# Kernel tuning notes

Hardware: AMD Instinct MI355X
Metric: run time of the kernel (lower is better)

Reference implementation:

```python
import jax, jax.numpy as jnp
import numpy as np
from jax import lax

B, P, E, A, D, EMB, V, L = 16, 196, 1024, 1024, 512, 512, 10000, 32
T = L - 1  # max decode steps


def setup_inputs() -> dict:
    key = jax.random.key(0)
    ks = jax.random.split(key, 24)

    def lin(k, fan_in, shape):
        return (jax.random.normal(k, shape, jnp.float32) / np.sqrt(fan_in)).astype(jnp.float32)

    inp = {}
    inp["encoder_out"] = jax.random.normal(ks[0], (B, P, E), jnp.float32)
    # Attention (note: original builds Attention(attention_dim, decoder_dim, attention_dim),
    # so encoder_att is Linear(A, A); works because E == A)
    inp["enc_att_W"] = lin(ks[1], A, (A, A))
    inp["enc_att_b"] = jnp.zeros((A,), jnp.float32)
    inp["dec_att_W"] = lin(ks[2], D, (D, A))
    inp["dec_att_b"] = jnp.zeros((A,), jnp.float32)
    inp["full_att_W"] = lin(ks[3], A, (A, 1))
    inp["full_att_b"] = jnp.zeros((1,), jnp.float32)
    # Embedding: uniform(-0.1, 0.1) per init_weights
    inp["emb"] = jax.random.uniform(ks[4], (V, EMB), jnp.float32, -0.1, 0.1)
    # LSTMCell(embed_dim + encoder_dim, decoder_dim): gate order i, f, g, o
    inp["W_ih"] = lin(ks[5], EMB + E, (EMB + E, 4 * D))
    inp["b_ih"] = jnp.zeros((4 * D,), jnp.float32)
    inp["W_hh"] = lin(ks[6], D, (D, 4 * D))
    inp["b_hh"] = jnp.zeros((4 * D,), jnp.float32)
    inp["init_h_W"] = lin(ks[7], E, (E, D))
    inp["init_h_b"] = jnp.zeros((D,), jnp.float32)
    inp["init_c_W"] = lin(ks[8], E, (E, D))
    inp["init_c_b"] = jnp.zeros((D,), jnp.float32)
    inp["f_beta_W"] = lin(ks[9], D, (D, E))
    inp["f_beta_b"] = jnp.zeros((E,), jnp.float32)
    # fc: weight uniform(-0.1, 0.1), bias 0 per init_weights
    inp["fc_W"] = jax.random.uniform(ks[10], (D, V), jnp.float32, -0.1, 0.1)
    inp["fc_b"] = jnp.zeros((V,), jnp.float32)
    inp["encoded_captions"] = jax.random.randint(ks[11], (B, L), 0, V, jnp.int32)
    lengths = jax.random.randint(ks[12], (B,), 2, L + 1, jnp.int32)
    lengths = lengths.at[0].set(L)  # guarantee max(decode_length) == L-1 (static T)
    inp["caption_length"] = lengths[:, None]
    return inp


def reference(encoder_out, enc_att_W, enc_att_b, dec_att_W, dec_att_b,
              full_att_W, full_att_b, emb, W_ih, b_ih, W_hh, b_hh,
              init_h_W, init_h_b, init_c_W, init_c_b,
              f_beta_W, f_beta_b, fc_W, fc_b,
              encoded_captions, caption_length):
    lengths = caption_length[:, 0]
    sort_ind = jnp.argsort(-lengths, stable=True)  # descending
    lengths_s = lengths[sort_ind]
    enc = encoder_out[sort_ind]                     # [B, P, E]
    caps = encoded_captions[sort_ind]               # [B, L]
    embs = emb[caps]                                # [B, L, EMB]
    decode_len = lengths_s - 1

    mean_enc = enc.mean(axis=1)
    h0 = mean_enc @ init_h_W + init_h_b             # [B, D]
    c0 = mean_enc @ init_c_W + init_c_b

    # encoder-side attention projection is h-independent; hoist out of the loop
    att1 = enc @ enc_att_W + enc_att_b              # [B, P, A]

    def step(carry, inp_t):
        h, c = carry
        emb_t, t = inp_t
        att2 = h @ dec_att_W + dec_att_b            # [B, A]
        att = (jax.nn.relu(att1 + att2[:, None, :]) @ full_att_W)[..., 0] + full_att_b[0]  # [B, P]
        alpha = jax.nn.softmax(att, axis=1)
        awe = jnp.einsum('bpe,bp->be', enc, alpha)  # [B, E]
        gate = jax.nn.sigmoid(h @ f_beta_W + f_beta_b)
        awe = gate + awe                            # NOTE: original uses '+' (not '*')
        x = jnp.concatenate([emb_t, awe], axis=1)   # [B, EMB+E]
        gates = x @ W_ih + b_ih + h @ W_hh + b_hh   # [B, 4D]
        i, f, g, o = jnp.split(gates, 4, axis=1)
        c_new = jax.nn.sigmoid(f) * c + jax.nn.sigmoid(i) * jnp.tanh(g)
        h_new = jax.nn.sigmoid(o) * jnp.tanh(c_new)
        active = (decode_len > t)[:, None]          # ragged batch mask (== [:batch_size_t])
        h2 = jnp.where(active, h_new, h)
        c2 = jnp.where(active, c_new, c)
        preds = h_new @ fc_W + fc_b                 # dropout in eval mode (identity)
        preds = jnp.where(active, preds, 0.0)
        alpha_m = jnp.where(active, alpha, 0.0)
        return (h2, c2), (preds, alpha_m)

    xs = (embs[:, :T].transpose(1, 0, 2), jnp.arange(T))
    _, (preds, alphas) = lax.scan(step, (h0, c0), xs)
    predictions = preds.transpose(1, 0, 2)          # [B, T, V]
    alphas = alphas.transpose(1, 0, 2)              # [B, T, P]
    return predictions, caps, decode_len, alphas, sort_ind
```

## Files before the change

kernel.cpp:

```cpp
#include <hip/hip_runtime.h>
#include <math.h>

#define NB 16
#define NP 196
#define NE 1024
#define ND 512
#define NEMB 512
#define NV 10000
#define NL 32
#define NT 31
#define NG 2048

#define NBLK 256

#define OFF_PRED    0
#define OFF_CAPS    4960000
#define OFF_DECLEN  4960512
#define OFF_ALPHAS  4960528
#define OFF_SORTIND 5057744

#define OFF_ATT1B   0
#define OFF_PREIHB  1605632
#define OFF_ENCT    2113536

#define WS_LEAF   64
#define WS_H      2304
#define WS_C      10496
#define WS_M1     18688
#define WS_SCORES 84224
#define WS_AWEG   88320
#define WS_HHIST  104704

#define SMEM_BYTES 82688

__device__ __forceinline__ float sigf(float x){ return 1.0f/(1.0f+expf(-x)); }
__device__ __forceinline__ unsigned short bf16rne(float x){
  unsigned u = __float_as_uint(x);
  unsigned r = (u + 0x7fffu + ((u>>16)&1u)) >> 16;
  return (unsigned short)r;
}
__device__ __forceinline__ float bf2f(unsigned short h){ return __uint_as_float(((unsigned)h)<<16); }
__device__ __forceinline__ void u2f2(unsigned u, float&a, float&b){
  a = __uint_as_float(u<<16); b = __uint_as_float(u & 0xffff0000u);
}
__device__ __forceinline__ void cstore(float* p, float v){
  __hip_atomic_store(p, v, __ATOMIC_RELAXED, __HIP_MEMORY_SCOPE_AGENT);
}
__device__ __forceinline__ float cload(const float* p){
  return __hip_atomic_load(p, __ATOMIC_RELAXED, __HIP_MEMORY_SCOPE_AGENT);
}
__device__ __forceinline__ float2 cload2(const float* p){
  unsigned long long u = __hip_atomic_load((const unsigned long long*)p, __ATOMIC_RELAXED, __HIP_MEMORY_SCOPE_AGENT);
  float2 r; r.x = __uint_as_float((unsigned)u); r.y = __uint_as_float((unsigned)(u>>32));
  return r;
}

__global__ void k_sort(const int* __restrict__ caplen, const int* __restrict__ caps,
                       int* __restrict__ wsi, float* __restrict__ out){
  __shared__ int sidx[NB];
  int tid = threadIdx.x;
  if (tid == 0){
    int len[NB], idx[NB];
    for (int i=0;i<NB;i++){ len[i]=caplen[i]; idx[i]=i; }
    for (int i=1;i<NB;i++){
      int key=idx[i]; int kl=len[key]; int j=i-1;
      while (j>=0 && len[idx[j]]<kl){ idx[j+1]=idx[j]; j--; }
      idx[j+1]=key;
    }
    for (int b=0;b<NB;b++){
      sidx[b]=idx[b];
      wsi[b]=idx[b];
      int dl = len[idx[b]]-1;
      wsi[NB+b]=dl;
      out[OFF_DECLEN+b]=(float)dl;
      out[OFF_SORTIND+b]=(float)idx[b];
    }
  }
  __syncthreads();
  for (int x = tid; x < 2304-64; x += 64) ((unsigned*)wsi)[WS_LEAF + x] = 0u;
  for (int x=tid; x<NB*NL; x+=blockDim.x){
    int b = x>>5, l = x&31;
    out[OFF_CAPS + x] = (float)caps[sidx[b]*NL + l];
  }
}

__global__ __launch_bounds__(256) void k_mean(const float* __restrict__ enc,
                                              const int* __restrict__ wsi,
                                              float* __restrict__ wsf){
  int gid = blockIdx.x*256 + threadIdx.x;
  int b = gid>>10, e = gid&1023;
  int ob = wsi[b];
  const float* p = enc + (size_t)ob*NP*NE + e;
  float s = 0.f;
  for (int i=0;i<NP;i++) s += p[(size_t)i*NE];
  wsf[WS_M1 + b*NE + e] = s*(1.0f/196.0f);
}

__global__ __launch_bounds__(256) void k_init(const float* __restrict__ ihW, const float* __restrict__ ihb,
                                              const float* __restrict__ icW, const float* __restrict__ icb,
                                              float* __restrict__ wsf){
  int gid = blockIdx.x*256 + threadIdx.x;
  int b = gid>>10, x = gid&1023;
  int d = x&511, which = x>>9;
  const float* W = which ? icW : ihW;
  const float* mp = wsf + WS_M1 + b*NE;
  float s = which ? icb[d] : ihb[d];
  for (int e=0;e<NE;e++) s = fmaf(mp[e], W[(size_t)e*ND + d], s);
  wsf[(which?WS_C:WS_H) + b*ND + d] = s;
}

__global__ __launch_bounds__(256) void k_trans(const float* __restrict__ enc,
                                               const int* __restrict__ wsi,
                                               unsigned short* __restrict__ encT){
  __shared__ float tile[196*65];
  const int tid = threadIdx.x;
  const int b = blockIdx.x >> 4, et = blockIdx.x & 15;
  const int e0 = et*64;
  const int ob = wsi[b];
  for (int idx = tid; idx < 196*16; idx += 256){
    int p = idx >> 4, q = idx & 15;
    float4 v = *(const float4*)(enc + (size_t)ob*NP*NE + (size_t)p*NE + e0 + q*4);
    tile[p*65 + q*4+0] = v.x; tile[p*65 + q*4+1] = v.y;
    tile[p*65 + q*4+2] = v.z; tile[p*65 + q*4+3] = v.w;
  }
  __syncthreads();
  for (int idx = tid; idx < 64*52; idx += 256){
    int el = idx/52, c = idx%52;
    ushort4 o;
    int p = c*4;
    o.x = (p+0<196) ? bf16rne(tile[(p+0)*65 + el]) : (unsigned short)0;
    o.y = (p+1<196) ? bf16rne(tile[(p+1)*65 + el]) : (unsigned short)0;
    o.z = (p+2<196) ? bf16rne(tile[(p+2)*65 + el]) : (unsigned short)0;
    o.w = (p+3<196) ? bf16rne(tile[(p+3)*65 + el]) : (unsigned short)0;
    *(ushort4*)(encT + ((size_t)(b*1024 + e0 + el))*208 + c*4) = o;
  }
}

__global__ __launch_bounds__(256) void k_gemm(const void* __restrict__ Abase,
                                              const float* __restrict__ Bmat,
                                              const float* __restrict__ bias1,
                                              const float* __restrict__ bias2,
                                              void* __restrict__ outv,
                                              int M, int N, int K, int mode,
                                              int abf16, int obf16,
                                              const int* __restrict__ wsi,
                                              const int* __restrict__ caps){
  __shared__ float As[16*64];
  __shared__ float Bs[16*64];
  int tid = threadIdx.x;
  int n0 = blockIdx.x*64, m0 = blockIdx.y*64;
  int tx = tid&15, ty = tid>>4;
  float acc[4][4] = {};
  int r = tid>>2, kq = tid&3;
  int kk = tid>>4, nq = tid&15;
  int row = m0 + r;
  const float* arow = nullptr;
  const unsigned short* arowu = nullptr;
  if (row < M){
    if (mode==0){ int b=row/196, p=row%196; arow = (const float*)Abase + (size_t)(wsi[b]*196 + p)*NE; }
    else if (mode==1){ int t=row>>4, b=row&15; int cap = caps[wsi[b]*NL + t]; arow = (const float*)Abase + (size_t)cap*NEMB; }
    else {
      if (abf16) arowu = (const unsigned short*)Abase + (size_t)row*K;
      else       arow  = (const float*)Abase + (size_t)row*K;
    }
  }
  int ktiles = K>>4;
  for (int kt=0; kt<ktiles; kt++){
    int k0 = kt<<4;
    float4 av = make_float4(0.f,0.f,0.f,0.f);
    if (arow) av = *(const float4*)(arow + k0 + kq*4);
    else if (arowu){
      ushort4 t = *(const ushort4*)(arowu + k0 + kq*4);
      av.x = bf2f(t.x); av.y = bf2f(t.y); av.z = bf2f(t.z); av.w = bf2f(t.w);
    }
    As[(kq*4+0)*64 + r] = av.x;
    As[(kq*4+1)*64 + r] = av.y;
    As[(kq*4+2)*64 + r] = av.z;
    As[(kq*4+3)*64 + r] = av.w;
    int ncol = n0 + nq*4;
    const float* bp = Bmat + (size_t)(k0+kk)*N + ncol;
    float4 bv;
    if (ncol+3 < N) bv = *(const float4*)bp;
    else {
      bv.x = (ncol+0<N)?bp[0]:0.f; bv.y = (ncol+1<N)?bp[1]:0.f;
      bv.z = (ncol+2<N)?bp[2]:0.f; bv.w = (ncol+3<N)?bp[3]:0.f;
    }
    *((float4*)&Bs[kk*64 + nq*4]) = bv;
    __syncthreads();
    #pragma unroll
    for (int k=0;k<16;k++){
      const float4 a = *(const float4*)(&As[k*64 + ty*4]);
      const float4 b = *(const float4*)(&Bs[k*64 + tx*4]);
      float ar[4] = {a.x,a.y,a.z,a.w};
      float br[4] = {b.x,b.y,b.z,b.w};
      #pragma unroll
      for (int i=0;i<4;i++)
        #pragma unroll
        for (int j=0;j<4;j++)
          acc[i][j] = fmaf(ar[i], br[j], acc[i][j]);
    }
    __syncthreads();
  }
  if (mode == 2){
    float* out = (float*)outv;
    #pragma unroll
    for (int i=0;i<4;i++){
      int m = m0 + ty*4 + i;
      if (m >= M) continue;
      int b = m & 15, t = m >> 4;
      bool act = wsi[NB + b] > t;
      size_t obase = (size_t)b*NT*NV + (size_t)t*NV;
      #pragma unroll
      for (int j=0;j<4;j++){
        int n = n0 + tx*4 + j;
        if (n >= N) continue;
        out[obase + n] = act ? (acc[i][j] + bias1[n]) : 0.0f;
      }
    }
  } else {
    #pragma unroll
    for (int i=0;i<4;i++){
      int m = m0 + ty*4 + i;
      if (m >= M) continue;
      #pragma unroll
      for (int j=0;j<4;j++){
        int n = n0 + tx*4 + j;
        if (n >= N) continue;
        float v = acc[i][j] + bias1[n];
        if (bias2) v += bias2[n];
        if (obf16) ((unsigned short*)outv)[(size_t)m*N + n] = bf16rne(v);
        else       ((float*)outv)[(size_t)m*N + n] = v;
      }
    }
  }
}

struct ScanParams {
  float* wsf;
  const int* wsi;
  const unsigned short* att1b;
  const unsigned short* preihb;
  const unsigned short* encT;
  const float* dec_att_W;
  const float* dec_att_b;
  const float* f_beta_W;
  const float* f_beta_b;
  const float* W_hh;
  const float* W_ih;
  const float* full_att_W;
  const float* full_att_b;
  float* out;
};

__device__ __forceinline__ void podbar(unsigned* base, int bxl, unsigned target){
  __syncthreads();
  if (threadIdx.x == 0){
    unsigned* lf = base + (bxl & 7)*32;
    unsigned a = __hip_atomic_fetch_add(lf, 1u, __ATOMIC_RELEASE, __HIP_MEMORY_SCOPE_AGENT);
    if (a == 7u){
      __hip_atomic_store(lf, 0u, __ATOMIC_RELAXED, __HIP_MEMORY_SCOPE_AGENT);
      unsigned r = __hip_atomic_fetch_add(base + 256, 1u, __ATOMIC_RELEASE, __HIP_MEMORY_SCOPE_AGENT);
      if (r == 7u){
        __hip_atomic_store(base + 256, 0u, __ATOMIC_RELAXED, __HIP_MEMORY_SCOPE_AGENT);
        __hip_atomic_fetch_add(base + 288, 1u, __ATOMIC_RELEASE, __HIP_MEMORY_SCOPE_AGENT);
      }
    }
    while ((int)(__hip_atomic_load(base + 288, __ATOMIC_RELAXED, __HIP_MEMORY_SCOPE_AGENT) - target) < 0)
      __builtin_amdgcn_s_sleep(1);
  }
  __syncthreads();
  __asm__ volatile("" ::: "memory");
}

__global__ __launch_bounds__(512, 2) void k_scan(ScanParams P){
  extern __shared__ __align__(16) unsigned char smem[];
  unsigned short* att1p = (unsigned short*)smem;
  unsigned short* encp  = (unsigned short*)(smem + 26624);
  float* uni     = (float*)(smem + 53504);
  float* scratch = (float*)(smem + 73984);

  const int tid = threadIdx.x;
  const int bx = blockIdx.x;
  const int pod = bx >> 6;
  const int bxl = bx & 63;
  const int B0 = pod*4;
  const int lane = tid & 63;
  const int wid = tid >> 6;

  float* M1     = P.wsf + WS_M1;
  float* hws    = P.wsf + WS_H;
  float* cws    = P.wsf + WS_C;
  float* scores = P.wsf + WS_SCORES;
  float* aweg   = P.wsf + WS_AWEG;
  unsigned short* hhist_us = (unsigned short*)(P.wsf + WS_HHIST);
  unsigned* bbase = (unsigned*)(P.wsf) + WS_LEAF + pod*320;
  const int* declen = P.wsi + NB;
  unsigned target = 0;

  const float* Wih2 = P.W_ih + (size_t)512*NG;
  const float fab = P.full_att_b[0];

  const int kcA = tid >> 6, cA = tid & 63;
  int modeA; const float* WAp; int jbA, ldwA;
  if (bxl < 16)      { WAp = P.dec_att_W; jbA = bxl*64;       ldwA = 1024; modeA = 0; }
  else if (bxl < 32) { WAp = P.f_beta_W;  jbA = (bxl-16)*64;  ldwA = 1024; modeA = 1; }
  else               { WAp = P.W_hh;      jbA = (bxl-32)*64;  ldwA = 2048; modeA = 2; }
  float wA[64];
  #pragma unroll
  for (int i=0;i<64;i++) wA[i] = WAp[(size_t)(kcA*64+i)*ldwA + jbA + cA];

  const int kcD = tid >> 5, cD = tid & 31;
  const int jD = (cD>>3)*512 + bxl*8 + (cD&7);
  float wD[64];
  #pragma unroll
  for (int i=0;i<64;i++) wD[i] = Wih2[(size_t)(kcD*64+i)*NG + jD];

  float faw[16];
  {
    const float* fw = P.full_att_W + lane*8;
    #pragma unroll
    for (int i=0;i<2;i++){
      float4 x = *(const float4*)(fw + i*512);
      float4 y = *(const float4*)(fw + i*512 + 4);
      faw[i*8+0]=x.x; faw[i*8+1]=x.y; faw[i*8+2]=x.z; faw[i*8+3]=x.w;
      faw[i*8+4]=y.x; faw[i*8+5]=y.y; faw[i*8+6]=y.z; faw[i*8+7]=y.w;
    }
  }

  {
    const int b = bx >> 4, sub = bx & 15;
    const int p0 = sub*13;
    const int cnt = (sub==15) ? 1 : 13;
    const uint4* s4 = (const uint4*)(P.att1b + ((size_t)(b*196 + p0))*1024);
    uint4* d4 = (uint4*)att1p;
    for (int i = tid; i < cnt*128; i += 512) d4[i] = s4[i];
    const unsigned* es = (const unsigned*)P.encT + (((size_t)(b*1024 + sub*64))*208 >> 1);
    unsigned* ed = (unsigned*)encp;
    for (int i = tid; i < 64*104; i += 512){
      int el = i/104, c = i%104;
      ed[el*105 + c] = es[el*104 + c];
    }
  }
  __syncthreads();

  float pa[4];

  for (int tt=0; tt<NT; tt++){
    if (declen[B0] <= tt){
      if ((bxl & 15) == 0){
        int b = B0 + (bxl >> 4);
        for (int t2 = tt; t2 < NT; t2++)
          for (int p = tid; p < NP; p += 512)
            P.out[OFF_ALPHAS + (size_t)b*NT*NP + (size_t)t2*NP + p] = 0.f;
      }
      break;
    }

    #pragma unroll
    for (int i=0;i<2;i++){
      int idx = tid + i*512;
      int b = idx >> 8, dp = (idx & 255)*2;
      float2 v = cload2(hws + (size_t)(B0+b)*ND + dp);
      int a = b*640 + (dp>>4)*20 + (dp&15);
      uni[a]   = v.x;
      uni[a+1] = v.y;
    }
    __syncthreads();

    {
      #pragma unroll
      for (int b=0;b<4;b++){
        float s = 0.f;
        #pragma unroll
        for (int cq=0;cq<4;cq++){
          const float4* hp = (const float4*)(uni + b*640 + kcA*80 + cq*20);
          float4 a0 = hp[0], a1 = hp[1], a2 = hp[2], a3 = hp[3];
          s = fmaf(a0.x,wA[cq*16+0],s);  s = fmaf(a0.y,wA[cq*16+1],s);  s = fmaf(a0.z,wA[cq*16+2],s);  s = fmaf(a0.w,wA[cq*16+3],s);
          s = fmaf(a1.x,wA[cq*16+4],s);  s = fmaf(a1.y,wA[cq*16+5],s);  s = fmaf(a1.z,wA[cq*16+6],s);  s = fmaf(a1.w,wA[cq*16+7],s);
          s = fmaf(a2.x,wA[cq*16+8],s);  s = fmaf(a2.y,wA[cq*16+9],s);  s = fmaf(a2.z,wA[cq*16+10],s); s = fmaf(a2.w,wA[cq*16+11],s);
          s = fmaf(a3.x,wA[cq*16+12],s); s = fmaf(a3.y,wA[cq*16+13],s); s = fmaf(a3.z,wA[cq*16+14],s); s = fmaf(a3.w,wA[cq*16+15],s);
        }
        pa[b] = s;
      }
      #pragma unroll
      for (int b=0;b<4;b++) scratch[kcA*256 + b*64 + cA] = pa[b];
      __syncthreads();
      if (tid < 256){
        float s = 0.f;
        #pragma unroll
        for (int w=0;w<8;w++) s += scratch[w*256 + tid];
        int b = tid >> 6, c = tid & 63;
        int jout = bxl*64 + c;
        float v;
        if (modeA==0)      v = s + P.dec_att_b[jout];
        else if (modeA==1) v = sigf(s + P.f_beta_b[jout-1024]);
        else               v = s;
        cstore(&M1[(size_t)(B0+b)*4096 + jout], v);
      }
    }
    podbar(bbase, bxl, ++target);

    {
      const int b = B0 + (bxl >> 4), sidx = bxl & 15;
      if (declen[b] > tt){
        float a2r[16];
        {
          const float* m1b = M1 + (size_t)b*4096 + lane*8;
          #pragma unroll
          for (int i=0;i<2;i++){
            #pragma unroll
            for (int q=0;q<4;q++){
              float2 t = cload2(m1b + i*512 + q*2);
              a2r[i*8+q*2]   = t.x;
              a2r[i*8+q*2+1] = t.y;
            }
          }
        }
        const int p0 = sidx*13;
        const int cnt = (sidx==15) ? 1 : 13;
        for (int rr = wid; rr < cnt; rr += 8){
          int p = p0 + rr;
          const unsigned short* a1 = att1p + (size_t)rr*1024;
          float s = 0.f;
          #pragma unroll
          for (int i=0;i<2;i++){
            uint4 u = *(const uint4*)(a1 + i*512 + lane*8);
            float f0,f1,v;
            u2f2(u.x,f0,f1);
            v = f0 + a2r[i*8+0]; v = v>0.f?v:0.f; s = fmaf(v, faw[i*8+0], s);
            v = f1 + a2r[i*8+1]; v = v>0.f?v:0.f; s = fmaf(v, faw[i*8+1], s);
            u2f2(u.y,f0,f1);
            v = f0 + a2r[i*8+2]; v = v>0.f?v:0.f; s = fmaf(v, faw[i*8+2], s);
            v = f1 + a2r[i*8+3]; v = v>0.f?v:0.f; s = fmaf(v, faw[i*8+3], s);
            u2f2(u.z,f0,f1);
            v = f0 + a2r[i*8+4]; v = v>0.f?v:0.f; s = fmaf(v, faw[i*8+4], s);
            v = f1 + a2r[i*8+5]; v = v>0.f?v:0.f; s = fmaf(v, faw[i*8+5], s);
            u2f2(u.w,f0,f1);
            v = f0 + a2r[i*8+6]; v = v>0.f?v:0.f; s = fmaf(v, faw[i*8+6], s);
            v = f1 + a2r[i*8+7]; v = v>0.f?v:0.f; s = fmaf(v, faw[i*8+7], s);
          }
          #pragma unroll
          for (int off=32; off; off>>=1) s += __shfl_down(s, off, 64);
          if (lane == 0) cstore(&scores[b*256 + p], s + fab);
        }
      }
    }
    podbar(bbase, bxl, ++target);

    {
      const int b = B0 + (bxl >> 4), ch = bxl & 15;
      if (declen[b] <= tt){
        if (ch == 0 && tid < 196)
          P.out[OFF_ALPHAS + (size_t)b*NT*NP + (size_t)tt*NP + tid] = 0.f;
      } else {
        float* sc   = scratch;
        float* red2 = scratch + 208;
        float* redp = scratch + 464;
        float v = (tid < 196) ? cload(&scores[b*256 + tid]) : -1e30f;
        if (tid < 208) sc[tid] = v;
        if (tid < 256) red2[tid] = v;
        __syncthreads();
        for (int s2=128; s2; s2>>=1){ if (tid < s2) red2[tid] = fmaxf(red2[tid], red2[tid+s2]); __syncthreads(); }
        const float mx = red2[0];
        __syncthreads();
        float ex = (tid < 196) ? expf(sc[tid] - mx) : 0.f;
        if (tid < 208) sc[tid] = ex;
        if (tid < 256) red2[tid] = ex;
        __syncthreads();
        for (int s2=128; s2; s2>>=1){ if (tid < s2) red2[tid] += red2[tid+s2]; __syncthreads(); }
        const float inv = 1.f / red2[0];
        __syncthreads();
        if (tid < 208) sc[tid] *= inv;
        __syncthreads();
        const int el = tid & 63, pp = tid >> 6;
        const unsigned* erowL = ((const unsigned*)encp) + el*105 + pp*13;
        float part = 0.f;
        #pragma unroll
        for (int i=0;i<13;i++){
          unsigned u = erowL[i];
          float f0,f1; u2f2(u,f0,f1);
          part = fmaf(f0, sc[pp*26 + 2*i],     part);
          part = fmaf(f1, sc[pp*26 + 2*i + 1], part);
        }
        redp[pp*68 + el] = part;
        __syncthreads();
        if (tid < 64){
          float aw = 0.f;
          #pragma unroll
          for (int q=0;q<8;q++) aw += redp[q*68 + tid];
          int e2 = ch*64 + tid;
          cstore(&aweg[b*1024 + e2], cload(&M1[(size_t)b*4096 + 1024 + e2]) + aw);
        }
        if (ch == 0 && tid < 196){
          P.out[OFF_ALPHAS + (size_t)b*NT*NP + (size_t)tt*NP + tid] = sc[tid];
        }
        __syncthreads();
      }
    }
    podbar(bbase, bxl, ++target);

    {
      #pragma unroll
      for (int i=0;i<4;i++){
        int idx = tid + i*512;
        int b = idx >> 9, ep = (idx & 511)*2;
        float2 v = cload2(aweg + (size_t)(B0+b)*1024 + ep);
        int a = b*1280 + (ep>>4)*20 + (ep&15);
        uni[a]   = v.x;
        uni[a+1] = v.y;
      }
      __syncthreads();
      #pragma unroll
      for (int b=0;b<4;b++){
        float s = 0.f;
        #pragma unroll
        for (int cq=0;cq<4;cq++){
          const float4* ap = (const float4*)(uni + b*1280 + kcD*80 + cq*20);
          float4 a0 = ap[0], a1 = ap[1], a2 = ap[2], a3 = ap[3];
          s = fmaf(a0.x,wD[cq*16+0],s);  s = fmaf(a0.y,wD[cq*16+1],s);  s = fmaf(a0.z,wD[cq*16+2],s);  s = fmaf(a0.w,wD[cq*16+3],s);
          s = fmaf(a1.x,wD[cq*16+4],s);  s = fmaf(a1.y,wD[cq*16+5],s);  s = fmaf(a1.z,wD[cq*16+6],s);  s = fmaf(a1.w,wD[cq*16+7],s);
          s = fmaf(a2.x,wD[cq*16+8],s);  s = fmaf(a2.y,wD[cq*16+9],s);  s = fmaf(a2.z,wD[cq*16+10],s); s = fmaf(a2.w,wD[cq*16+11],s);
          s = fmaf(a3.x,wD[cq*16+12],s); s = fmaf(a3.y,wD[cq*16+13],s); s = fmaf(a3.z,wD[cq*16+14],s); s = fmaf(a3.w,wD[cq*16+15],s);
        }
        pa[b] = s;
      }
      #pragma unroll
      for (int b=0;b<4;b++) scratch[kcD*128 + b*32 + cD] = pa[b];
      __syncthreads();
      float* gl = scratch + 2048;
      if (tid < 128){
        float s = 0.f;
        #pragma unroll
        for (int w=0;w<16;w++) s += scratch[w*128 + tid];
        int c = tid & 31, b = tid >> 5;
        int j = (c>>3)*512 + bxl*8 + (c&7);
        int B = B0 + b;
        float gv = s + bf2f(P.preihb[(size_t)(tt*NB + B)*NG + j]) + cload(&M1[(size_t)B*4096 + 2048 + j]);
        gl[b*32 + c] = gv;
      }
      __syncthreads();
      if (tid < 32){
        const int b = tid >> 3, dq = tid & 7;
        const int B = B0 + b, d = bxl*8 + dq;
        const float gI = gl[b*32 + 0  + dq];
        const float gF = gl[b*32 + 8  + dq];
        const float gG = gl[b*32 + 16 + dq];
        const float gO = gl[b*32 + 24 + dq];
        const float co = cws[(size_t)B*ND + d];
        const float cn = sigf(gF)*co + sigf(gI)*tanhf(gG);
        const float hn = sigf(gO)*tanhf(cn);
        hhist_us[((size_t)tt*NB + B)*ND + d] = bf16rne(hn);
        if (declen[B] > tt){
          cstore(&hws[(size_t)B*ND + d], hn);
          cws[(size_t)B*ND + d] = cn;
        }
      }
      __syncthreads();
    }
    podbar(bbase, bxl, ++target);
  }
}

extern "C" void kernel_launch(void* const* d_in, const int* in_sizes, int n_in,
                              void* d_out, int out_size, void* d_ws, size_t ws_size,
                              hipStream_t stream) {
  const float* encoder_out = (const float*)d_in[0];
  const float* enc_att_W   = (const float*)d_in[1];
  const float* enc_att_b   = (const float*)d_in[2];
  const float* dec_att_W   = (const float*)d_in[3];
  const float* dec_att_b   = (const float*)d_in[4];
  const float* full_att_W  = (const float*)d_in[5];
  const float* full_att_b  = (const float*)d_in[6];
  const float* emb         = (const float*)d_in[7];
  const float* W_ih        = (const float*)d_in[8];
  const float* b_ih        = (const float*)d_in[9];
  const float* W_hh        = (const float*)d_in[10];
  const float* b_hh        = (const float*)d_in[11];
  const float* init_h_W    = (const float*)d_in[12];
  const float* init_h_b    = (const float*)d_in[13];
  const float* init_c_W    = (const float*)d_in[14];
  const float* init_c_b    = (const float*)d_in[15];
  const float* f_beta_W    = (const float*)d_in[16];
  const float* f_beta_b    = (const float*)d_in[17];
  const float* fc_W        = (const float*)d_in[18];
  const float* fc_b        = (const float*)d_in[19];
  const int*   caps        = (const int*)d_in[20];
  const int*   caplen      = (const int*)d_in[21];
  (void)in_sizes; (void)n_in; (void)out_size; (void)ws_size;

  float* out = (float*)d_out;
  float* wsf = (float*)d_ws;
  int*   wsi = (int*)d_ws;
  unsigned short* att1b  = (unsigned short*)(out + OFF_ATT1B);
  unsigned short* preihb = (unsigned short*)(out + OFF_PREIHB);
  unsigned short* encT   = (unsigned short*)(out + OFF_ENCT);

  hipFuncSetAttribute((const void*)k_scan, hipFuncAttributeMaxDynamicSharedMemorySize, SMEM_BYTES);

  hipLaunchKernelGGL(k_sort, dim3(1), dim3(64), 0, stream, caplen, caps, wsi, out);
  hipLaunchKernelGGL(k_mean, dim3(64), dim3(256), 0, stream, encoder_out, wsi, wsf);
  hipLaunchKernelGGL(k_init, dim3(64), dim3(256), 0, stream, init_h_W, init_h_b, init_c_W, init_c_b, wsf);
  hipLaunchKernelGGL(k_trans, dim3(256), dim3(256), 0, stream, encoder_out, wsi, encT);
  hipLaunchKernelGGL(k_gemm, dim3(16,49), dim3(256), 0, stream,
                     (const void*)encoder_out, enc_att_W, enc_att_b, (const float*)nullptr,
                     (void*)att1b, 3136, 1024, 1024, 0, 0, 1, wsi, caps);
  hipLaunchKernelGGL(k_gemm, dim3(32,8), dim3(256), 0, stream,
                     (const void*)emb, W_ih, b_ih, b_hh,
                     (void*)preihb, 496, 2048, 512, 1, 0, 1, wsi, caps);

  ScanParams sp;
  sp.wsf = wsf; sp.wsi = wsi;
  sp.att1b = att1b; sp.preihb = preihb; sp.encT = encT;
  sp.dec_att_W = dec_att_W; sp.dec_att_b = dec_att_b;
  sp.f_beta_W = f_beta_W; sp.f_beta_b = f_beta_b;
  sp.W_hh = W_hh; sp.W_ih = W_ih;
  sp.full_att_W = full_att_W; sp.full_att_b = full_att_b;
  sp.out = out;
  void* args[] = { &sp };
  hipLaunchCooperativeKernel((void*)k_scan, dim3(NBLK), dim3(512), args, SMEM_BYTES, stream);

  hipLaunchKernelGGL(k_gemm, dim3(157,8), dim3(256), 0, stream,
                     (const void*)(wsf + WS_HHIST), fc_W, fc_b, (const float*)nullptr,
                     (void*)out, 496, 10000, 512, 2, 1, 0, wsi, caps);
}
```

Baseline: 1.228 ms.

## Skip inactive FC tiles, use wave-shuffle softmax, prefetch gate bias early

The final FC GEMM now orders its rows batch-major (b*NT+t), and k_sort precomputes per 64-row block flags so that fully inactive row blocks write zeros and skip the matmul. The attention softmax replaces the shared-memory tree reductions with wavefront shuffle reductions, which removes many __syncthreads. The LSTM gate pre-activation term (M1 plus preihb) is loaded before the attention phase so its latency is hidden. This relies on the sorted ragged lengths to find empty blocks and changes the row indexing in the FC epilogue.

```diff
diff --git a/kernel.cpp b/kernel.cpp
--- a/kernel.cpp
+++ b/kernel.cpp
@@ -67,13 +67,22 @@
       while (j>=0 && len[idx[j]]<kl){ idx[j+1]=idx[j]; j--; }
       idx[j+1]=key;
     }
+    int dl[NB];
     for (int b=0;b<NB;b++){
       sidx[b]=idx[b];
       wsi[b]=idx[b];
-      int dl = len[idx[b]]-1;
-      wsi[NB+b]=dl;
-      out[OFF_DECLEN+b]=(float)dl;
+      dl[b] = len[idx[b]]-1;
+      wsi[NB+b]=dl[b];
+      out[OFF_DECLEN+b]=(float)dl[b];
       out[OFF_SORTIND+b]=(float)idx[b];
+    }
+    for (int mb=0; mb<8; mb++){
+      int any = 0;
+      for (int m=mb*64; m<mb*64+64 && m<NB*NT; m++){
+        int b = m/NT, t = m - b*NT;
+        if (t < dl[b]) any = 1;
+      }
+      wsi[32+mb] = any;
     }
   }
   __syncthreads();
@@ -150,6 +159,22 @@
   int tid = threadIdx.x;
   int n0 = blockIdx.x*64, m0 = blockIdx.y*64;
   int tx = tid&15, ty = tid>>4;
+  if (mode==2 && wsi[32 + blockIdx.y] == 0){
+    float* outp = (float*)outv;
+    #pragma unroll
+    for (int i=0;i<4;i++){
+      int m = m0 + ty*4 + i;
+      if (m >= M) continue;
+      int b = m/NT, t = m - b*NT;
+      size_t obase = (size_t)b*NT*NV + (size_t)t*NV;
+      #pragma unroll
+      for (int j=0;j<4;j++){
+        int n = n0 + tx*4 + j;
+        if (n < N) outp[obase + n] = 0.0f;
+      }
+    }
+    return;
+  }
   float acc[4][4] = {};
   int r = tid>>2, kq = tid&3;
   int kk = tid>>4, nq = tid&15;
@@ -160,8 +185,9 @@
     if (mode==0){ int b=row/196, p=row%196; arow = (const float*)Abase + (size_t)(wsi[b]*196 + p)*NE; }
     else if (mode==1){ int t=row>>4, b=row&15; int cap = caps[wsi[b]*NL + t]; arow = (const float*)Abase + (size_t)cap*NEMB; }
     else {
-      if (abf16) arowu = (const unsigned short*)Abase + (size_t)row*K;
-      else       arow  = (const float*)Abase + (size_t)row*K;
+      int b = row/NT, t = row - b*NT;
+      if (abf16) arowu = (const unsigned short*)Abase + (size_t)(t*NB + b)*K;
+      else       arow  = (const float*)Abase + (size_t)(t*NB + b)*K;
     }
   }
   int ktiles = K>>4;
@@ -207,7 +233,7 @@
     for (int i=0;i<4;i++){
       int m = m0 + ty*4 + i;
       if (m >= M) continue;
-      int b = m & 15, t = m >> 4;
+      int b = m/NT, t = m - b*NT;
       bool act = wsi[NB + b] > t;
       size_t obase = (size_t)b*NT*NV + (size_t)t*NV;
       #pragma unroll
@@ -399,6 +425,14 @@
       }
     }
     podbar(bbase, bxl, ++target);
+
+    float gpre = 0.f;
+    if (tid < 128){
+      const int cQ = tid & 31, bQ = tid >> 5;
+      const int jQ = (cQ>>3)*512 + bxl*8 + (cQ&7);
+      const int BQ = B0 + bQ;
+      gpre = cload(&M1[(size_t)BQ*4096 + 2048 + jQ]) + bf2f(P.preihb[(size_t)(tt*NB + BQ)*NG + jQ]);
+    }
 
     {
       const int b = B0 + (bxl >> 4), sidx = bxl & 15;
@@ -454,23 +488,28 @@
           P.out[OFF_ALPHAS + (size_t)b*NT*NP + (size_t)tt*NP + tid] = 0.f;
       } else {
         float* sc   = scratch;
-        float* red2 = scratch + 208;
+        float* wred = scratch + 208;
         float* redp = scratch + 464;
         float v = (tid < 196) ? cload(&scores[b*256 + tid]) : -1e30f;
-        if (tid < 208) sc[tid] = v;
-        if (tid < 256) red2[tid] = v;
+        float mw = v;
+        #pragma unroll
+        for (int off=32; off; off>>=1) mw = fmaxf(mw, __shfl_xor(mw, off, 64));
+        if (lane == 0) wred[wid] = mw;
         __syncthreads();
-        for (int s2=128; s2; s2>>=1){ if (tid < s2) red2[tid] = fmaxf(red2[tid], red2[tid+s2]); __syncthreads(); }
-        const float mx = red2[0];
+        float mx = wred[0];
+        #pragma unroll
+        for (int w=1;w<8;w++) mx = fmaxf(mx, wred[w]);
+        float ex = (tid < 196) ? expf(v - mx) : 0.f;
+        float sm = ex;
+        #pragma unroll
+        for (int off=32; off; off>>=1) sm += __shfl_xor(sm, off, 64);
+        if (lane == 0) wred[8+wid] = sm;
         __syncthreads();
-        float ex = (tid < 196) ? expf(sc[tid] - mx) : 0.f;
-        if (tid < 208) sc[tid] = ex;
-        if (tid < 256) red2[tid] = ex;
-        __syncthreads();
-        for (int s2=128; s2; s2>>=1){ if (tid < s2) red2[tid] += red2[tid+s2]; __syncthreads(); }
-        const float inv = 1.f / red2[0];
-        __syncthreads();
-        if (tid < 208) sc[tid] *= inv;
+        float tot = wred[8];
+        #pragma unroll
+        for (int w=1;w<8;w++) tot += wred[8+w];
+        const float inv = 1.f / tot;
+        if (tid < 208) sc[tid] = (tid < 196) ? ex*inv : 0.f;
         __syncthreads();
         const int el = tid & 63, pp = tid >> 6;
         const unsigned* erowL = ((const unsigned*)encp) + el*105 + pp*13;
@@ -533,9 +572,7 @@
         #pragma unroll
         for (int w=0;w<16;w++) s += scratch[w*128 + tid];
         int c = tid & 31, b = tid >> 5;
-        int j = (c>>3)*512 + bxl*8 + (c&7);
-        int B = B0 + b;
-        float gv = s + bf2f(P.preihb[(size_t)(tt*NB + B)*NG + j]) + cload(&M1[(size_t)B*4096 + 2048 + j]);
+        float gv = s + gpre;
         gl[b*32 + c] = gv;
       }
       __syncthreads();
```

Result: faster. 1.193 ms (-2.9%).
